# Kernel tuning notes

Measured on AMD Instinct MI355X. Metric: run time of the kernel, lower is better.

## Reference

```python
import jax, jax.numpy as jnp
import numpy as np

N = 50000      # nodes
E = 800000     # edges (no self loops; added in reference like PyG add_self_loops)
IN = 128       # in_channel
C = 64         # out_channel
K = 64         # cos_num (correlation embedding dim)
H = 1          # heads
NEG_SLOPE = 0.2


def setup_inputs() -> dict:
    key = jax.random.key(0)
    ks = jax.random.split(key, 10)
    x = jax.random.normal(ks[0], (N, IN), dtype=jnp.float32)
    corrs = jax.random.normal(ks[1], (N, K), dtype=jnp.float32)
    # random edges guaranteed to have src != dst (original remove_self_loops)
    src = jax.random.randint(ks[2], (E,), 0, N)
    off = jax.random.randint(ks[3], (E,), 1, N)
    dst = (src + off) % N
    edge_index = jnp.stack([src, dst]).astype(jnp.int32)  # [2, E]
    W = jax.random.normal(ks[4], (IN, H * C), dtype=jnp.float32) / np.sqrt(IN)
    att_i = jax.random.normal(ks[5], (1, H, C), dtype=jnp.float32) * 0.1
    att_j = jax.random.normal(ks[6], (1, H, C), dtype=jnp.float32) * 0.1
    att_em_i = jax.random.normal(ks[7], (1, H, K), dtype=jnp.float32) * 0.1
    att_em_j = jax.random.normal(ks[8], (1, H, K), dtype=jnp.float32) * 0.1
    bias = jnp.zeros((C,), dtype=jnp.float32)
    return {"x": x, "edge_index": edge_index, "corrs": corrs, "W": W,
            "att_i": att_i, "att_j": att_j,
            "att_em_i": att_em_i, "att_em_j": att_em_j, "bias": bias}


def reference(x, edge_index, corrs, W, att_i, att_j, att_em_i, att_em_j, bias):
    # add self loops (original: remove_self_loops then add_self_loops)
    loops = jnp.arange(N, dtype=edge_index.dtype)
    src = jnp.concatenate([edge_index[0], loops])   # [E+N] message sources (x_j)
    dst = jnp.concatenate([edge_index[1], loops])   # [E+N] message targets (x_i)

    g = (x @ W).reshape(N, H, C)                    # linear projection, [N,H,C]
    gj = g[src]                                     # source features per edge [E+N,H,C]
    gi = g[dst]                                     # target features per edge
    ej = corrs[src][:, None, :]                     # [E+N,1,K] broadcast over heads
    ei = corrs[dst][:, None, :]

    # GAT-style score on concatenated key [g || corr]
    alpha = (jnp.sum(gi * att_i, -1) + jnp.sum(ei * att_em_i, -1)
             + jnp.sum(gj * att_j, -1) + jnp.sum(ej * att_em_j, -1))   # [E+N,H]
    alpha = jax.nn.leaky_relu(alpha, NEG_SLOPE)

    # neighbor softmax over incoming edges of each target node (per head)
    amax = jax.ops.segment_max(alpha, dst, num_segments=N)
    ex = jnp.exp(alpha - amax[dst])
    denom = jax.ops.segment_sum(ex, dst, num_segments=N)
    a = ex / (denom[dst] + 1e-16)                   # [E+N,H]

    # scatter-add weighted messages
    out = jax.ops.segment_sum(gj * a[..., None], dst, num_segments=N)  # [N,H,C]
    out = out.mean(axis=1) + bias                    # concat=False -> head mean

    # wrapper: float cast + ReLU
    return jax.nn.relu(out.astype(jnp.float32))
```

## Files before the change

### kernel.cpp

```cpp
#include <hip/hip_runtime.h>
#include <hip/hip_bf16.h>
#include <math.h>

#define IN_DIM 128
#define C_DIM 64
#define BKT_CHUNK 4096

typedef short bf16x8 __attribute__((ext_vector_type(8)));
typedef float f32x4 __attribute__((ext_vector_type(4)));

static __device__ __forceinline__ unsigned short f2bf(float f) {
    unsigned int u = __float_as_uint(f);
    u += 0x7FFFu + ((u >> 16) & 1u);
    return (unsigned short)(u >> 16);
}
static __device__ __forceinline__ float bf2f(unsigned short h) {
    return __uint_as_float(((unsigned int)h) << 16);
}

__global__ __launch_bounds__(256) void k_gemm_bucket(
    const float* __restrict__ x, const float* __restrict__ W,
    const float* __restrict__ corrs,
    const float* __restrict__ att_i, const float* __restrict__ att_j,
    const float* __restrict__ att_em_i, const float* __restrict__ att_em_j,
    unsigned short* __restrict__ g_bf, float* __restrict__ s_i, float* __restrict__ s_j,
    int N, int GB,
    const int* __restrict__ src, const int* __restrict__ dst,
    int E, int NB, int CAP,
    int* __restrict__ bucket_cnt, unsigned int* __restrict__ staging)
{
    __shared__ __attribute__((aligned(16))) unsigned short WT[2][64][128];
    __shared__ int cnt[256];
    __shared__ int run[256];
    __shared__ int cur[256];

    int tid = threadIdx.x;

    if (blockIdx.x >= GB) {
        cnt[tid] = 0;
        __syncthreads();

        int T = E + N;
        int base = (blockIdx.x - GB) * BKT_CHUNK;
#pragma unroll
        for (int k = 0; k < BKT_CHUNK / 256; ++k) {
            int i = base + k * 256 + tid;
            if (i < T) {
                int d = (i < E) ? dst[i] : (i - E);
                atomicAdd(&cnt[d >> 8], 1);
            }
        }
        __syncthreads();
        if (tid < NB && cnt[tid] > 0) run[tid] = atomicAdd(&bucket_cnt[tid], cnt[tid]);
        cur[tid] = 0;
        __syncthreads();
#pragma unroll
        for (int k = 0; k < BKT_CHUNK / 256; ++k) {
            int i = base + k * 256 + tid;
            if (i < T) {
                int d, s;
                if (i < E) { d = dst[i]; s = src[i]; }
                else       { d = i - E; s = d; }
                int b = d >> 8;
                int ofs = atomicAdd(&cur[b], 1);
                int pos = run[b] + ofs;
                if (pos < CAP)
                    staging[(size_t)b * CAP + pos] =
                        (unsigned)s | ((unsigned)(d & 255) << 16);
            }
        }
        return;
    }

#pragma unroll
    for (int p = 0; p < 8; ++p) {
        int f = p * 1024 + tid * 4;
        f32x4 w4 = *(const f32x4*)(W + f);
        int k  = f >> 6;
        int c0 = f & 63;
#pragma unroll
        for (int i = 0; i < 4; ++i) {
            int c = c0 + i;
            float wv = w4[i];
            unsigned short hi = f2bf(wv);
            unsigned short lo = f2bf(wv - bf2f(hi));
            int ks = k ^ ((c & 7) << 3);
            WT[0][c][ks] = hi;
            WT[1][c][ks] = lo;
        }
    }
    __syncthreads();

    int wv = tid >> 6, lane = tid & 63;
    int mrow = lane & 15;
    int kgrp = lane >> 4;
    int row  = blockIdx.x * 64 + wv * 16 + mrow;
    int rowc = min(row, N - 1);

    f32x4 acc[4];
#pragma unroll
    for (int t = 0; t < 4; ++t) { f32x4 z = {0.f, 0.f, 0.f, 0.f}; acc[t] = z; }

    f32x4 xa[4], xb[4];
#pragma unroll
    for (int s = 0; s < 4; ++s) {
        const float* xp = x + (size_t)rowc * IN_DIM + s * 32 + kgrp * 8;
        xa[s] = *(const f32x4*)xp;
        xb[s] = *(const f32x4*)(xp + 4);
    }

#pragma unroll
    for (int s = 0; s < 4; ++s) {
        bf16x8 ah;
#pragma unroll
        for (int i = 0; i < 4; ++i) {
            ah[i]     = (short)f2bf(xa[s][i]);
            ah[4 + i] = (short)f2bf(xb[s][i]);
        }
        int kbase = s * 32 + kgrp * 8;
#pragma unroll
        for (int t = 0; t < 4; ++t) {
            int c  = t * 16 + mrow;
            int ks = kbase ^ ((c & 7) << 3);
            bf16x8 bh = *(const bf16x8*)&WT[0][c][ks];
            bf16x8 bl = *(const bf16x8*)&WT[1][c][ks];
            acc[t] = __builtin_amdgcn_mfma_f32_16x16x32_bf16(ah, bh, acc[t], 0, 0, 0);
            acc[t] = __builtin_amdgcn_mfma_f32_16x16x32_bf16(ah, bl, acc[t], 0, 0, 0);
        }
    }

    float ai[4], aj[4], aei[4], aej[4];
#pragma unroll
    for (int t = 0; t < 4; ++t) {
        ai[t]  = att_i[t * 16 + mrow];
        aj[t]  = att_j[t * 16 + mrow];
        aei[t] = att_em_i[t * 16 + mrow];
        aej[t] = att_em_j[t * 16 + mrow];
    }
    int crow_base = blockIdx.x * 64 + wv * 16 + (lane >> 4) * 4;
#pragma unroll
    for (int r = 0; r < 4; ++r) {
        int grow  = crow_base + r;
        int growc = min(grow, N - 1);
        float vi = 0.f, vj = 0.f;
        ushort4 hv;
#pragma unroll
        for (int t = 0; t < 4; ++t) {
            float gv = acc[t][r];
            float cv = corrs[(size_t)growc * 64 + t * 16 + mrow];
            unsigned short h = f2bf(gv);
            if (t == 0) hv.x = h; else if (t == 1) hv.y = h;
            else if (t == 2) hv.z = h; else hv.w = h;
            vi = fmaf(gv, ai[t], fmaf(cv, aei[t], vi));
            vj = fmaf(gv, aj[t], fmaf(cv, aej[t], vj));
        }
        if (grow < N)
            *(ushort4*)(g_bf + (size_t)grow * C_DIM + mrow * 4) = hv;
#pragma unroll
        for (int o = 1; o < 16; o <<= 1) {
            vi += __shfl_xor(vi, o);
            vj += __shfl_xor(vj, o);
        }
        if (mrow == 0 && grow < N) { s_i[grow] = vi; s_j[grow] = vj; }
    }
}

__global__ __launch_bounds__(256) void k_scatter(
    const unsigned int* __restrict__ staging, const int* __restrict__ bucket_cnt,
    int N, int CAP,
    const float* __restrict__ s_i, const float* __restrict__ s_j,
    int* __restrict__ row_start, int* __restrict__ row_end,
    unsigned int* __restrict__ edge_rec)
{
    __shared__ int cnt[256];
    __shared__ int off[257];
    __shared__ int cur[256];
    __shared__ int wsum[4];
    __shared__ float si_l[256];

    int b = blockIdx.x, t = threadIdx.x;
    int lo = b << 8;
    int hi = min(lo + 256, N);
    int bcnt = min(bucket_cnt[b], CAP);
    const unsigned int* sb = staging + (size_t)b * CAP;

    cnt[t] = 0;
    if (lo + t < N) si_l[t] = s_i[lo + t];
    __syncthreads();

    for (int r = t; r < bcnt; r += 256)
        atomicAdd(&cnt[(sb[r] >> 16) & 255], 1);
    __syncthreads();

    int s = cnt[t];
    int lane = t & 63, wv = t >> 6;
    int incl = s;
#pragma unroll
    for (int o = 1; o < 64; o <<= 1) {
        int u = __shfl_up(incl, o);
        if (lane >= o) incl += u;
    }
    if (lane == 63) wsum[wv] = incl;
    __syncthreads();
    int woff = 0;
    for (int w = 0; w < wv; ++w) woff += wsum[w];
    int ex = woff + incl - s;
    off[t] = ex;
    cur[t] = ex;
    if (t == 255) off[256] = woff + incl;
    __syncthreads();

    int rawb = b * CAP;
    for (int i = t; i < hi - lo; i += 256) {
        row_start[lo + i] = rawb + off[i];
        row_end[lo + i]   = rawb + off[i + 1];
    }
    for (int r = t; r < bcnt; r += 256) {
        unsigned int rec = sb[r];
        int dl   = (rec >> 16) & 255;
        int srcn = rec & 0xFFFFu;
        float a = si_l[dl] + s_j[srcn];
        a = (a > 0.f) ? a : 0.2f * a;
        float w = __expf(a);
        int slot = atomicAdd(&cur[dl], 1);
        edge_rec[rawb + slot] = ((unsigned)f2bf(w) << 16) | (unsigned)srcn;
    }
}

__global__ __launch_bounds__(256) void k_aggregate(
    const unsigned short* __restrict__ g_bf,
    const int* __restrict__ row_start, const int* __restrict__ row_end,
    const unsigned int* __restrict__ edge_rec,
    const float* __restrict__ bias, float* __restrict__ out, int N)
{
    int wave = threadIdx.x >> 6, lane = threadIdx.x & 63;
    int n = blockIdx.x * 4 + wave;
    if (n >= N) return;

    int start = row_start[n];
    int end   = row_end[n];

    int grp = lane >> 3;
    int cl  = lane & 7;
    float a0 = 0.f, a1 = 0.f, a2 = 0.f, a3 = 0.f;
    float a4 = 0.f, a5 = 0.f, a6 = 0.f, a7 = 0.f, den = 0.f;
#pragma unroll 2
    for (int e0 = start; e0 < end; e0 += 8) {
        int e = e0 + grp;
        if (e < end) {
            unsigned int rec = edge_rec[e];
            int   srcn = rec & 0xFFFFu;
            float w    = bf2f((unsigned short)(rec >> 16));
            const ushort4* gp = (const ushort4*)(g_bf + (size_t)srcn * C_DIM + (cl << 3));
            ushort4 g0 = gp[0];
            ushort4 g1 = gp[1];
            a0 = fmaf(w, bf2f(g0.x), a0);
            a1 = fmaf(w, bf2f(g0.y), a1);
            a2 = fmaf(w, bf2f(g0.z), a2);
            a3 = fmaf(w, bf2f(g0.w), a3);
            a4 = fmaf(w, bf2f(g1.x), a4);
            a5 = fmaf(w, bf2f(g1.y), a5);
            a6 = fmaf(w, bf2f(g1.z), a6);
            a7 = fmaf(w, bf2f(g1.w), a7);
            den += w;
        }
    }
#pragma unroll
    for (int o = 8; o < 64; o <<= 1) {
        a0  += __shfl_xor(a0, o);
        a1  += __shfl_xor(a1, o);
        a2  += __shfl_xor(a2, o);
        a3  += __shfl_xor(a3, o);
        a4  += __shfl_xor(a4, o);
        a5  += __shfl_xor(a5, o);
        a6  += __shfl_xor(a6, o);
        a7  += __shfl_xor(a7, o);
        den += __shfl_xor(den, o);
    }
    if (grp == 0) {
        float inv = 1.f / (den + 1e-16f);
        float av[8] = {a0, a1, a2, a3, a4, a5, a6, a7};
        float* op = out + (size_t)n * C_DIM;
#pragma unroll
        for (int j = 0; j < 8; ++j) {
            int p  = (cl << 3) + j;
            int ch = ((p & 3) << 4) + (p >> 2);
            op[ch] = fmaxf(fmaf(av[j], inv, bias[ch]), 0.f);
        }
    }
}

extern "C" void kernel_launch(void* const* d_in, const int* in_sizes, int n_in,
                              void* d_out, int out_size, void* d_ws, size_t ws_size,
                              hipStream_t stream)
{
    const float* x        = (const float*)d_in[0];
    const int*   eidx     = (const int*)  d_in[1];
    const float* corrs    = (const float*)d_in[2];
    const float* W        = (const float*)d_in[3];
    const float* att_i    = (const float*)d_in[4];
    const float* att_j    = (const float*)d_in[5];
    const float* att_em_i = (const float*)d_in[6];
    const float* att_em_j = (const float*)d_in[7];
    const float* bias     = (const float*)d_in[8];
    float* out = (float*)d_out;

    int N = in_sizes[0] / IN_DIM;
    int E = in_sizes[1] / 2;
    const int* src = eidx;
    const int* dst = eidx + E;

    int T  = E + N;
    int NB = (N + 255) >> 8;
    int CAP = ((T + NB - 1) / NB);
    CAP = CAP + CAP / 4;
    CAP = (CAP + 63) & ~63;

    char* ws = (char*)d_ws;
    size_t off = 0;
    auto alloc = [&](size_t bytes) -> void* {
        void* p = ws + off;
        off += (bytes + 255) & ~(size_t)255;
        return p;
    };
    unsigned short* g_bf = (unsigned short*)alloc((size_t)N * C_DIM * sizeof(unsigned short));
    float* s_i       = (float*)alloc((size_t)N * sizeof(float));
    float* s_j       = (float*)alloc((size_t)N * sizeof(float));
    unsigned int* staging  = (unsigned int*)alloc((size_t)NB * CAP * sizeof(unsigned int));
    unsigned int* edge_rec = (unsigned int*)alloc((size_t)NB * CAP * sizeof(unsigned int));
    int*   row_start = (int*)alloc((size_t)N * sizeof(int));
    int*   row_end   = (int*)alloc((size_t)N * sizeof(int));
    int*   bucket_cnt= (int*)alloc(256 * sizeof(int));
    (void)ws_size; (void)n_in; (void)out_size;

    hipMemsetAsync(bucket_cnt, 0, 256 * sizeof(int), stream);

    int GB = (N + 63) / 64;
    int BB = (T + BKT_CHUNK - 1) / BKT_CHUNK;
    k_gemm_bucket<<<GB + BB, 256, 0, stream>>>(
        x, W, corrs, att_i, att_j, att_em_i, att_em_j, g_bf, s_i, s_j,
        N, GB, src, dst, E, NB, CAP, bucket_cnt, staging);

    k_scatter<<<NB, 256, 0, stream>>>(
        staging, bucket_cnt, N, CAP, s_i, s_j, row_start, row_end, edge_rec);

    k_aggregate<<<(N + 3) / 4, 256, 0, stream>>>(
        g_bf, row_start, row_end, edge_rec, bias, out, N);
}
```

Measured before the change: 75.32 us.

## Fuse scatter and aggregate into one kernel with 64-node buckets in LDS

Shrinks dst buckets from 256 to 64 nodes so each bucket's edges fit in shared memory. Scatter (CSR build plus edge-weight computation) and aggregation are merged into one kernel that keeps the sorted edge records in LDS, which removes the global edge_rec and row_start/row_end round trip and one kernel launch. The GEMM blocks now process 128 rows each and the bucketing chunks double in size. Capping CAP at 1440 risks silently dropping edges if a bucket overflows, and the fused kernel launches fewer, longer blocks for the aggregation phase.

```diff
diff --git a/kernel.cpp b/kernel.cpp
--- a/kernel.cpp
+++ b/kernel.cpp
@@ -4,7 +4,9 @@
 
 #define IN_DIM 128
 #define C_DIM 64
-#define BKT_CHUNK 4096
+#define BKT_CHUNK 8192
+#define BS 64
+#define SA_CAP 1440
 
 typedef short bf16x8 __attribute__((ext_vector_type(8)));
 typedef float f32x4 __attribute__((ext_vector_type(4)));
@@ -30,14 +32,14 @@
     int* __restrict__ bucket_cnt, unsigned int* __restrict__ staging)
 {
     __shared__ __attribute__((aligned(16))) unsigned short WT[2][64][128];
-    __shared__ int cnt[256];
-    __shared__ int run[256];
-    __shared__ int cur[256];
+    __shared__ int cnt[1024];
+    __shared__ int run[1024];
+    __shared__ int cur[1024];
 
     int tid = threadIdx.x;
 
     if (blockIdx.x >= GB) {
-        cnt[tid] = 0;
+        for (int i = tid; i < NB; i += 256) cnt[i] = 0;
         __syncthreads();
 
         int T = E + N;
@@ -47,12 +49,14 @@
             int i = base + k * 256 + tid;
             if (i < T) {
                 int d = (i < E) ? dst[i] : (i - E);
-                atomicAdd(&cnt[d >> 8], 1);
+                atomicAdd(&cnt[d >> 6], 1);
             }
         }
         __syncthreads();
-        if (tid < NB && cnt[tid] > 0) run[tid] = atomicAdd(&bucket_cnt[tid], cnt[tid]);
-        cur[tid] = 0;
+        for (int i = tid; i < NB; i += 256) {
+            cur[i] = 0;
+            if (cnt[i] > 0) run[i] = atomicAdd(&bucket_cnt[i], cnt[i]);
+        }
         __syncthreads();
 #pragma unroll
         for (int k = 0; k < BKT_CHUNK / 256; ++k) {
@@ -61,12 +65,12 @@
                 int d, s;
                 if (i < E) { d = dst[i]; s = src[i]; }
                 else       { d = i - E; s = d; }
-                int b = d >> 8;
+                int b = d >> 6;
                 int ofs = atomicAdd(&cur[b], 1);
                 int pos = run[b] + ofs;
                 if (pos < CAP)
                     staging[(size_t)b * CAP + pos] =
-                        (unsigned)s | ((unsigned)(d & 255) << 16);
+                        (unsigned)s | ((unsigned)(d & 63) << 16);
             }
         }
         return;
@@ -94,40 +98,6 @@
     int wv = tid >> 6, lane = tid & 63;
     int mrow = lane & 15;
     int kgrp = lane >> 4;
-    int row  = blockIdx.x * 64 + wv * 16 + mrow;
-    int rowc = min(row, N - 1);
-
-    f32x4 acc[4];
-#pragma unroll
-    for (int t = 0; t < 4; ++t) { f32x4 z = {0.f, 0.f, 0.f, 0.f}; acc[t] = z; }
-
-    f32x4 xa[4], xb[4];
-#pragma unroll
-    for (int s = 0; s < 4; ++s) {
-        const float* xp = x + (size_t)rowc * IN_DIM + s * 32 + kgrp * 8;
-        xa[s] = *(const f32x4*)xp;
-        xb[s] = *(const f32x4*)(xp + 4);
-    }
-
-#pragma unroll
-    for (int s = 0; s < 4; ++s) {
-        bf16x8 ah;
-#pragma unroll
-        for (int i = 0; i < 4; ++i) {
-            ah[i]     = (short)f2bf(xa[s][i]);
-            ah[4 + i] = (short)f2bf(xb[s][i]);
-        }
-        int kbase = s * 32 + kgrp * 8;
-#pragma unroll
-        for (int t = 0; t < 4; ++t) {
-            int c  = t * 16 + mrow;
-            int ks = kbase ^ ((c & 7) << 3);
-            bf16x8 bh = *(const bf16x8*)&WT[0][c][ks];
-            bf16x8 bl = *(const bf16x8*)&WT[1][c][ks];
-            acc[t] = __builtin_amdgcn_mfma_f32_16x16x32_bf16(ah, bh, acc[t], 0, 0, 0);
-            acc[t] = __builtin_amdgcn_mfma_f32_16x16x32_bf16(ah, bl, acc[t], 0, 0, 0);
-        }
-    }
 
     float ai[4], aj[4], aei[4], aej[4];
 #pragma unroll
@@ -137,155 +107,182 @@
         aei[t] = att_em_i[t * 16 + mrow];
         aej[t] = att_em_j[t * 16 + mrow];
     }
-    int crow_base = blockIdx.x * 64 + wv * 16 + (lane >> 4) * 4;
-#pragma unroll
-    for (int r = 0; r < 4; ++r) {
-        int grow  = crow_base + r;
-        int growc = min(grow, N - 1);
-        float vi = 0.f, vj = 0.f;
-        ushort4 hv;
-#pragma unroll
-        for (int t = 0; t < 4; ++t) {
-            float gv = acc[t][r];
-            float cv = corrs[(size_t)growc * 64 + t * 16 + mrow];
-            unsigned short h = f2bf(gv);
-            if (t == 0) hv.x = h; else if (t == 1) hv.y = h;
-            else if (t == 2) hv.z = h; else hv.w = h;
-            vi = fmaf(gv, ai[t], fmaf(cv, aei[t], vi));
-            vj = fmaf(gv, aj[t], fmaf(cv, aej[t], vj));
-        }
-        if (grow < N)
-            *(ushort4*)(g_bf + (size_t)grow * C_DIM + mrow * 4) = hv;
-#pragma unroll
-        for (int o = 1; o < 16; o <<= 1) {
-            vi += __shfl_xor(vi, o);
-            vj += __shfl_xor(vj, o);
-        }
-        if (mrow == 0 && grow < N) { s_i[grow] = vi; s_j[grow] = vj; }
-    }
-}
-
-__global__ __launch_bounds__(256) void k_scatter(
+
+    for (int half = 0; half < 2; ++half) {
+        int row = blockIdx.x * 128 + half * 64 + wv * 16 + mrow;
+        int rowc = min(row, N - 1);
+
+        f32x4 acc[4];
+#pragma unroll
+        for (int t = 0; t < 4; ++t) { f32x4 z = {0.f, 0.f, 0.f, 0.f}; acc[t] = z; }
+
+        f32x4 xa[4], xb[4];
+#pragma unroll
+        for (int s = 0; s < 4; ++s) {
+            const float* xp = x + (size_t)rowc * IN_DIM + s * 32 + kgrp * 8;
+            xa[s] = *(const f32x4*)xp;
+            xb[s] = *(const f32x4*)(xp + 4);
+        }
+
+#pragma unroll
+        for (int s = 0; s < 4; ++s) {
+            bf16x8 ah;
+#pragma unroll
+            for (int i = 0; i < 4; ++i) {
+                ah[i]     = (short)f2bf(xa[s][i]);
+                ah[4 + i] = (short)f2bf(xb[s][i]);
+            }
+            int kbase = s * 32 + kgrp * 8;
+#pragma unroll
+            for (int t = 0; t < 4; ++t) {
+                int c  = t * 16 + mrow;
+                int ks = kbase ^ ((c & 7) << 3);
+                bf16x8 bh = *(const bf16x8*)&WT[0][c][ks];
+                bf16x8 bl = *(const bf16x8*)&WT[1][c][ks];
+                acc[t] = __builtin_amdgcn_mfma_f32_16x16x32_bf16(ah, bh, acc[t], 0, 0, 0);
+                acc[t] = __builtin_amdgcn_mfma_f32_16x16x32_bf16(ah, bl, acc[t], 0, 0, 0);
+            }
+        }
+
+        int crow_base = blockIdx.x * 128 + half * 64 + wv * 16 + (lane >> 4) * 4;
+#pragma unroll
+        for (int r = 0; r < 4; ++r) {
+            int grow  = crow_base + r;
+            int growc = min(grow, N - 1);
+            float vi = 0.f, vj = 0.f;
+            ushort4 hv;
+#pragma unroll
+            for (int t = 0; t < 4; ++t) {
+                float gv = acc[t][r];
+                float cv = corrs[(size_t)growc * 64 + t * 16 + mrow];
+                unsigned short h = f2bf(gv);
+                if (t == 0) hv.x = h; else if (t == 1) hv.y = h;
+                else if (t == 2) hv.z = h; else hv.w = h;
+                vi = fmaf(gv, ai[t], fmaf(cv, aei[t], vi));
+                vj = fmaf(gv, aj[t], fmaf(cv, aej[t], vj));
+            }
+            if (grow < N)
+                *(ushort4*)(g_bf + (size_t)grow * C_DIM + mrow * 4) = hv;
+#pragma unroll
+            for (int o = 1; o < 16; o <<= 1) {
+                vi += __shfl_xor(vi, o);
+                vj += __shfl_xor(vj, o);
+            }
+            if (mrow == 0 && grow < N) { s_i[grow] = vi; s_j[grow] = vj; }
+        }
+    }
+}
+
+__global__ __launch_bounds__(256) void k_scatter_agg(
     const unsigned int* __restrict__ staging, const int* __restrict__ bucket_cnt,
     int N, int CAP,
     const float* __restrict__ s_i, const float* __restrict__ s_j,
-    int* __restrict__ row_start, int* __restrict__ row_end,
-    unsigned int* __restrict__ edge_rec)
+    const unsigned short* __restrict__ g_bf,
+    const float* __restrict__ bias, float* __restrict__ out)
 {
-    __shared__ int cnt[256];
-    __shared__ int off[257];
-    __shared__ int cur[256];
-    __shared__ int wsum[4];
-    __shared__ float si_l[256];
-
-    int b = blockIdx.x, t = threadIdx.x;
-    int lo = b << 8;
-    int hi = min(lo + 256, N);
+    __shared__ unsigned int raw[SA_CAP];
+    __shared__ unsigned int wrecs[SA_CAP];
+    __shared__ int   cnt[BS];
+    __shared__ int   off[BS + 1];
+    __shared__ int   cur[BS];
+    __shared__ float si_l[BS];
+
+    int b = blockIdx.x, tid = threadIdx.x;
+    int lo = b * BS;
     int bcnt = min(bucket_cnt[b], CAP);
     const unsigned int* sb = staging + (size_t)b * CAP;
 
-    cnt[t] = 0;
-    if (lo + t < N) si_l[t] = s_i[lo + t];
-    __syncthreads();
-
-    for (int r = t; r < bcnt; r += 256)
-        atomicAdd(&cnt[(sb[r] >> 16) & 255], 1);
-    __syncthreads();
-
-    int s = cnt[t];
-    int lane = t & 63, wv = t >> 6;
-    int incl = s;
-#pragma unroll
-    for (int o = 1; o < 64; o <<= 1) {
-        int u = __shfl_up(incl, o);
-        if (lane >= o) incl += u;
-    }
-    if (lane == 63) wsum[wv] = incl;
-    __syncthreads();
-    int woff = 0;
-    for (int w = 0; w < wv; ++w) woff += wsum[w];
-    int ex = woff + incl - s;
-    off[t] = ex;
-    cur[t] = ex;
-    if (t == 255) off[256] = woff + incl;
-    __syncthreads();
-
-    int rawb = b * CAP;
-    for (int i = t; i < hi - lo; i += 256) {
-        row_start[lo + i] = rawb + off[i];
-        row_end[lo + i]   = rawb + off[i + 1];
-    }
-    for (int r = t; r < bcnt; r += 256) {
-        unsigned int rec = sb[r];
-        int dl   = (rec >> 16) & 255;
+    for (int r = tid; r < bcnt; r += 256) raw[r] = sb[r];
+    if (tid < BS) {
+        cnt[tid] = 0;
+        si_l[tid] = (lo + tid < N) ? s_i[lo + tid] : 0.f;
+    }
+    __syncthreads();
+
+    for (int r = tid; r < bcnt; r += 256)
+        atomicAdd(&cnt[(raw[r] >> 16) & 63], 1);
+    __syncthreads();
+
+    if (tid < 64) {
+        int s = cnt[tid];
+        int incl = s;
+#pragma unroll
+        for (int o = 1; o < 64; o <<= 1) {
+            int u = __shfl_up(incl, o);
+            if (tid >= o) incl += u;
+        }
+        off[tid] = incl - s;
+        cur[tid] = incl - s;
+        if (tid == 63) off[64] = incl;
+    }
+    __syncthreads();
+
+    for (int r = tid; r < bcnt; r += 256) {
+        unsigned int rec = raw[r];
+        int dl   = (rec >> 16) & 63;
         int srcn = rec & 0xFFFFu;
         float a = si_l[dl] + s_j[srcn];
         a = (a > 0.f) ? a : 0.2f * a;
         float w = __expf(a);
         int slot = atomicAdd(&cur[dl], 1);
-        edge_rec[rawb + slot] = ((unsigned)f2bf(w) << 16) | (unsigned)srcn;
-    }
-}
-
-__global__ __launch_bounds__(256) void k_aggregate(
-    const unsigned short* __restrict__ g_bf,
-    const int* __restrict__ row_start, const int* __restrict__ row_end,
-    const unsigned int* __restrict__ edge_rec,
-    const float* __restrict__ bias, float* __restrict__ out, int N)
-{
-    int wave = threadIdx.x >> 6, lane = threadIdx.x & 63;
-    int n = blockIdx.x * 4 + wave;
-    if (n >= N) return;
-
-    int start = row_start[n];
-    int end   = row_end[n];
-
+        wrecs[slot] = ((unsigned)f2bf(w) << 16) | (unsigned)srcn;
+    }
+    __syncthreads();
+
+    int wave = tid >> 6, lane = tid & 63;
     int grp = lane >> 3;
     int cl  = lane & 7;
-    float a0 = 0.f, a1 = 0.f, a2 = 0.f, a3 = 0.f;
-    float a4 = 0.f, a5 = 0.f, a6 = 0.f, a7 = 0.f, den = 0.f;
+    for (int nl = wave; nl < BS; nl += 4) {
+        int n = lo + nl;
+        if (n >= N) break;
+        int start = off[nl];
+        int end   = off[nl + 1];
+
+        float a0 = 0.f, a1 = 0.f, a2 = 0.f, a3 = 0.f;
+        float a4 = 0.f, a5 = 0.f, a6 = 0.f, a7 = 0.f, den = 0.f;
 #pragma unroll 2
-    for (int e0 = start; e0 < end; e0 += 8) {
-        int e = e0 + grp;
-        if (e < end) {
-            unsigned int rec = edge_rec[e];
-            int   srcn = rec & 0xFFFFu;
-            float w    = bf2f((unsigned short)(rec >> 16));
-            const ushort4* gp = (const ushort4*)(g_bf + (size_t)srcn * C_DIM + (cl << 3));
-            ushort4 g0 = gp[0];
-            ushort4 g1 = gp[1];
-            a0 = fmaf(w, bf2f(g0.x), a0);
-            a1 = fmaf(w, bf2f(g0.y), a1);
-            a2 = fmaf(w, bf2f(g0.z), a2);
-            a3 = fmaf(w, bf2f(g0.w), a3);
-            a4 = fmaf(w, bf2f(g1.x), a4);
-            a5 = fmaf(w, bf2f(g1.y), a5);
-            a6 = fmaf(w, bf2f(g1.z), a6);
-            a7 = fmaf(w, bf2f(g1.w), a7);
-            den += w;
-        }
-    }
-#pragma unroll
-    for (int o = 8; o < 64; o <<= 1) {
-        a0  += __shfl_xor(a0, o);
-        a1  += __shfl_xor(a1, o);
-        a2  += __shfl_xor(a2, o);
-        a3  += __shfl_xor(a3, o);
-        a4  += __shfl_xor(a4, o);
-        a5  += __shfl_xor(a5, o);
-        a6  += __shfl_xor(a6, o);
-        a7  += __shfl_xor(a7, o);
-        den += __shfl_xor(den, o);
-    }
-    if (grp == 0) {
-        float inv = 1.f / (den + 1e-16f);
-        float av[8] = {a0, a1, a2, a3, a4, a5, a6, a7};
-        float* op = out + (size_t)n * C_DIM;
-#pragma unroll
-        for (int j = 0; j < 8; ++j) {
-            int p  = (cl << 3) + j;
-            int ch = ((p & 3) << 4) + (p >> 2);
-            op[ch] = fmaxf(fmaf(av[j], inv, bias[ch]), 0.f);
+        for (int e0 = start; e0 < end; e0 += 8) {
+            int e = e0 + grp;
+            if (e < end) {
+                unsigned int rec = wrecs[e];
+                int   srcn = rec & 0xFFFFu;
+                float w    = bf2f((unsigned short)(rec >> 16));
+                const ushort4* gp = (const ushort4*)(g_bf + (size_t)srcn * C_DIM + (cl << 3));
+                ushort4 g0 = gp[0];
+                ushort4 g1 = gp[1];
+                a0 = fmaf(w, bf2f(g0.x), a0);
+                a1 = fmaf(w, bf2f(g0.y), a1);
+                a2 = fmaf(w, bf2f(g0.z), a2);
+                a3 = fmaf(w, bf2f(g0.w), a3);
+                a4 = fmaf(w, bf2f(g1.x), a4);
+                a5 = fmaf(w, bf2f(g1.y), a5);
+                a6 = fmaf(w, bf2f(g1.z), a6);
+                a7 = fmaf(w, bf2f(g1.w), a7);
+                den += w;
+            }
+        }
+#pragma unroll
+        for (int o = 8; o < 64; o <<= 1) {
+            a0  += __shfl_xor(a0, o);
+            a1  += __shfl_xor(a1, o);
+            a2  += __shfl_xor(a2, o);
+            a3  += __shfl_xor(a3, o);
+            a4  += __shfl_xor(a4, o);
+            a5  += __shfl_xor(a5, o);
+            a6  += __shfl_xor(a6, o);
+            a7  += __shfl_xor(a7, o);
+            den += __shfl_xor(den, o);
+        }
+        if (grp == 0) {
+            float inv = 1.f / (den + 1e-16f);
+            float av[8] = {a0, a1, a2, a3, a4, a5, a6, a7};
+            float* op = out + (size_t)n * C_DIM;
+#pragma unroll
+            for (int j = 0; j < 8; ++j) {
+                int p  = (cl << 3) + j;
+                int ch = ((p & 3) << 4) + (p >> 2);
+                op[ch] = fmaxf(fmaf(av[j], inv, bias[ch]), 0.f);
+            }
         }
     }
 }
@@ -311,10 +308,11 @@
     const int* dst = eidx + E;
 
     int T  = E + N;
-    int NB = (N + 255) >> 8;
+    int NB = (N + BS - 1) / BS;
     int CAP = ((T + NB - 1) / NB);
     CAP = CAP + CAP / 4;
     CAP = (CAP + 63) & ~63;
+    if (CAP > SA_CAP) CAP = SA_CAP;
 
     char* ws = (char*)d_ws;
     size_t off = 0;
@@ -326,24 +324,18 @@
     unsigned short* g_bf = (unsigned short*)alloc((size_t)N * C_DIM * sizeof(unsigned short));
     float* s_i       = (float*)alloc((size_t)N * sizeof(float));
     float* s_j       = (float*)alloc((size_t)N * sizeof(float));
-    unsigned int* staging  = (unsigned int*)alloc((size_t)NB * CAP * sizeof(unsigned int));
-    unsigned int* edge_rec = (unsigned int*)alloc((size_t)NB * CAP * sizeof(unsigned int));
-    int*   row_start = (int*)alloc((size_t)N * sizeof(int));
-    int*   row_end   = (int*)alloc((size_t)N * sizeof(int));
-    int*   bucket_cnt= (int*)alloc(256 * sizeof(int));
+    unsigned int* staging = (unsigned int*)alloc((size_t)NB * CAP * sizeof(unsigned int));
+    int*   bucket_cnt= (int*)alloc((size_t)1024 * sizeof(int));
     (void)ws_size; (void)n_in; (void)out_size;
 
-    hipMemsetAsync(bucket_cnt, 0, 256 * sizeof(int), stream);
-
-    int GB = (N + 63) / 64;
+    hipMemsetAsync(bucket_cnt, 0, 1024 * sizeof(int), stream);
+
+    int GB = (N + 127) / 128;
     int BB = (T + BKT_CHUNK - 1) / BKT_CHUNK;
     k_gemm_bucket<<<GB + BB, 256, 0, stream>>>(
         x, W, corrs, att_i, att_j, att_em_i, att_em_j, g_bf, s_i, s_j,
         N, GB, src, dst, E, NB, CAP, bucket_cnt, staging);
 
-    k_scatter<<<NB, 256, 0, stream>>>(
-        staging, bucket_cnt, N, CAP, s_i, s_j, row_start, row_end, edge_rec);
-
-    k_aggregate<<<(N + 3) / 4, 256, 0, stream>>>(
-        g_bf, row_start, row_end, edge_rec, bias, out, N);
-}
+    k_scatter_agg<<<NB, 256, 0, stream>>>(
+        staging, bucket_cnt, N, CAP, s_i, s_j, g_bf, bias, out);
+}
```

Measured after the change: 83.01 us. 1.1x slower.
